# Optimization experiments

Measured on AMD Instinct MI355X. Metric: run time of the kernel, lower is better.

The kernel has to match this reference:

```python
import jax, jax.numpy as jnp
import numpy as np

EPS = 1e-16

def setup_inputs() -> dict:
    key = jax.random.key(0)
    k1, k2 = jax.random.split(key)
    lhs = jax.random.uniform(k1, (100000, 2), dtype=jnp.float32)
    rhs = jax.random.uniform(k2, (512, 2), dtype=jnp.float32)
    return {"lhs": lhs, "rhs": rhs}

def reference(lhs, rhs):
    # lhs: [N,2] (w,h), rhs: [M,2] (w,h) -> IoU matrix [N,M]
    lw, lh = lhs[:, 0:1], lhs[:, 1:2]          # [N,1]
    rw, rh = rhs[None, :, 0], rhs[None, :, 1]  # [1,M]
    intersection = jnp.minimum(lw, rw) * jnp.minimum(lh, rh)   # [N,M]
    union = lw * lh + rw * rh - intersection                    # [N,M]
    return intersection / union + EPS
```

## Files before the change

kernel.cpp:

```cpp
#include <hip/hip_runtime.h>


#define NCOLS 512

typedef float vfloat4 __attribute__((ext_vector_type(4)));

__global__ __launch_bounds__(256) void iou_kernel(
    const float2* __restrict__ lhs,
    const float*  __restrict__ rhs,
    float* __restrict__ out,
    int n_rows, int total_waves)
{
    const int tid  = blockIdx.x * blockDim.x + threadIdx.x;
    const int lane = threadIdx.x & 63;
    const int wave = __builtin_amdgcn_readfirstlane(tid >> 6);

    const vfloat4* rhs4 = (const vfloat4*)rhs;
    vfloat4 a0 = rhs4[2 * lane];
    vfloat4 a1 = rhs4[2 * lane + 1];
    vfloat4 b0 = rhs4[128 + 2 * lane];
    vfloat4 b1 = rhs4[128 + 2 * lane + 1];

    float rw[8] = {a0.x, a0.z, a1.x, a1.z, b0.x, b0.z, b1.x, b1.z};
    float rh[8] = {a0.y, a0.w, a1.y, a1.w, b0.y, b0.w, b1.y, b1.w};
    float ra[8];
#pragma unroll
    for (int k = 0; k < 8; ++k) ra[k] = rw[k] * rh[k];

    for (int row = wave; row < n_rows; row += total_waves) {
        float2 l = lhs[row];
        float la = l.x * l.y;

        float o[8];
#pragma unroll
        for (int k = 0; k < 8; ++k) {
            float inter = fminf(l.x, rw[k]) * fminf(l.y, rh[k]);
            float uni   = (la + ra[k]) - inter;
            o[k] = fmaf(inter, __builtin_amdgcn_rcpf(uni), 1e-16f);
        }

        vfloat4* orow = (vfloat4*)(out + (size_t)row * NCOLS);
        vfloat4 v0 = {o[0], o[1], o[2], o[3]};
        vfloat4 v1 = {o[4], o[5], o[6], o[7]};
        orow[lane]      = v0;
        orow[64 + lane] = v1;
    }
}

extern "C" void kernel_launch(void* const* d_in, const int* in_sizes, int n_in,
                              void* d_out, int out_size, void* d_ws, size_t ws_size,
                              hipStream_t stream) {
    const float2* lhs = (const float2*)d_in[0];
    const float*  rhs = (const float*)d_in[1];
    float* out = (float*)d_out;

    int n_rows = in_sizes[0] / 2;

    int blocks = 2048;
    int total_waves = blocks * (256 / 64);
    iou_kernel<<<blocks, 256, 0, stream>>>(lhs, rhs, out, n_rows, total_waves);
}
```

Measured before the change: 202.2 us.

## Process fixed row groups per wave with all lhs loads issued upfront

```diff
diff --git a/kernel.cpp b/kernel.cpp
--- a/kernel.cpp
+++ b/kernel.cpp
@@ -2,6 +2,8 @@
 
 
 #define NCOLS 512
+#define RPB 4
+#define KITERS 3
 
 typedef float vfloat4 __attribute__((ext_vector_type(4)));
 
@@ -9,11 +11,11 @@
     const float2* __restrict__ lhs,
     const float*  __restrict__ rhs,
     float* __restrict__ out,
-    int n_rows, int total_waves)
+    int n_blocks, int total_waves)
 {
-    const int tid  = blockIdx.x * blockDim.x + threadIdx.x;
     const int lane = threadIdx.x & 63;
-    const int wave = __builtin_amdgcn_readfirstlane(tid >> 6);
+    const int wave = __builtin_amdgcn_readfirstlane(
+        (int)(blockIdx.x * blockDim.x + threadIdx.x) >> 6);
 
     const vfloat4* rhs4 = (const vfloat4*)rhs;
     vfloat4 a0 = rhs4[2 * lane];
@@ -27,23 +29,39 @@
 #pragma unroll
     for (int k = 0; k < 8; ++k) ra[k] = rw[k] * rh[k];
 
-    for (int row = wave; row < n_rows; row += total_waves) {
-        float2 l = lhs[row];
-        float la = l.x * l.y;
+    int blk[KITERS];
+#pragma unroll
+    for (int k = 0; k < KITERS; ++k) {
+        int b = wave + k * total_waves;
+        blk[k] = (b < n_blocks) ? b : (n_blocks - 1);
+    }
 
-        float o[8];
+    float2 l[KITERS][RPB];
 #pragma unroll
-        for (int k = 0; k < 8; ++k) {
-            float inter = fminf(l.x, rw[k]) * fminf(l.y, rh[k]);
-            float uni   = (la + ra[k]) - inter;
-            o[k] = fmaf(inter, __builtin_amdgcn_rcpf(uni), 1e-16f);
+    for (int k = 0; k < KITERS; ++k)
+#pragma unroll
+        for (int r = 0; r < RPB; ++r)
+            l[k][r] = lhs[blk[k] * RPB + r];
+
+#pragma unroll
+    for (int k = 0; k < KITERS; ++k) {
+        vfloat4* obase = (vfloat4*)(out + (size_t)blk[k] * RPB * NCOLS);
+#pragma unroll
+        for (int r = 0; r < RPB; ++r) {
+            const float lw = l[k][r].x, lh = l[k][r].y;
+            const float la = lw * lh;
+            float o[8];
+#pragma unroll
+            for (int j = 0; j < 8; ++j) {
+                float inter = fminf(lw, rw[j]) * fminf(lh, rh[j]);
+                float uni   = (la + ra[j]) - inter;
+                o[j] = fmaf(inter, __builtin_amdgcn_rcpf(uni), 1e-16f);
+            }
+            vfloat4 v0 = {o[0], o[1], o[2], o[3]};
+            vfloat4 v1 = {o[4], o[5], o[6], o[7]};
+            obase[r * 128 + lane]      = v0;
+            obase[r * 128 + 64 + lane] = v1;
         }
-
-        vfloat4* orow = (vfloat4*)(out + (size_t)row * NCOLS);
-        vfloat4 v0 = {o[0], o[1], o[2], o[3]};
-        vfloat4 v1 = {o[4], o[5], o[6], o[7]};
-        orow[lane]      = v0;
-        orow[64 + lane] = v1;
     }
 }
 
@@ -54,9 +72,12 @@
     const float*  rhs = (const float*)d_in[1];
     float* out = (float*)d_out;
 
-    int n_rows = in_sizes[0] / 2;
+    int n_rows   = in_sizes[0] / 2;
+    int n_blocks = (n_rows + RPB - 1) / RPB;
 
-    int blocks = 2048;
-    int total_waves = blocks * (256 / 64);
-    iou_kernel<<<blocks, 256, 0, stream>>>(lhs, rhs, out, n_rows, total_waves);
+    int waves_needed = (n_blocks + KITERS - 1) / KITERS;
+    int blocks = (waves_needed + 3) / 4;
+    int total_waves = blocks * 4;
+
+    iou_kernel<<<blocks, 256, 0, stream>>>(lhs, rhs, out, n_blocks, total_waves);
 }
```

Result: no change. 199.9 us (-1.2%).
